# Performance work log

Hardware: AMD Instinct MI355X
Metric: run time of the kernel (lower is better)

Reference implementation:

```python
import jax, jax.numpy as jnp
import numpy as np
from jax import lax

C = 64          # in_c
D_INNER = 128   # expand=2 * C
D_STATE = 16
D_CONV = 4
DT_RANK = 4     # ceil(C/16)
B, H, W = 4, 64, 64


def setup_inputs() -> dict:
    key = jax.random.key(0)
    ks = jax.random.split(key, 22)
    def n(k, shape, s=0.05):
        return jax.random.normal(k, shape, jnp.float32) * s
    inp = {}
    inp["x"] = jax.random.normal(ks[0], (B, C, H, W), jnp.float32)
    # AxialDW: depthwise (3,1) and (1,3) convs, groups=C
    inp["dwh_w"] = n(ks[1], (C, 1, 3, 1), 0.2); inp["dwh_b"] = n(ks[2], (C,))
    inp["dww_w"] = n(ks[3], (C, 1, 1, 3), 0.2); inp["dww_b"] = n(ks[4], (C,))
    # 1x1 conv
    inp["conv_w"] = n(ks[5], (C, C, 1, 1), 0.1); inp["conv_b"] = n(ks[6], (C,))
    # BatchNorm (eval mode, running stats)
    inp["bn_g"] = jnp.ones((C,), jnp.float32); inp["bn_b"] = jnp.zeros((C,), jnp.float32)
    inp["bn_m"] = n(ks[7], (C,), 0.1)
    inp["bn_v"] = jnp.abs(n(ks[8], (C,), 0.1)) + 1.0
    # ResMambaBlock: LayerNorm + Mamba(d_model=C) + residual
    inp["ln_g"] = jnp.ones((C,), jnp.float32); inp["ln_b"] = jnp.zeros((C,), jnp.float32)
    inp["in_proj_w"] = n(ks[9], (2 * D_INNER, C))
    inp["convd_w"] = n(ks[10], (D_INNER, 1, D_CONV), 0.2); inp["convd_b"] = n(ks[11], (D_INNER,))
    inp["x_proj_w"] = n(ks[12], (DT_RANK + 2 * D_STATE, D_INNER))
    inp["dt_proj_w"] = n(ks[13], (D_INNER, DT_RANK), 0.2)
    inp["dt_proj_b"] = n(ks[14], (D_INNER,), 0.5) - 4.0  # softplus -> small dt
    inp["A_log"] = jnp.log(jnp.tile(jnp.arange(1, D_STATE + 1, dtype=jnp.float32), (D_INNER, 1)))
    inp["Dp"] = jnp.ones((D_INNER,), jnp.float32)
    inp["out_proj_w"] = n(ks[15], (C, D_INNER))
    return inp


def _mamba(h, in_proj_w, convd_w, convd_b, x_proj_w, dt_proj_w, dt_proj_b, A_log, Dp, out_proj_w):
    # h: [B, L, C]
    Bt, L, _ = h.shape
    xz = jnp.einsum('blc,dc->bld', h, in_proj_w)          # [B,L,2*D_INNER]
    xm, z = jnp.split(xz, 2, axis=-1)
    # causal depthwise conv1d over L
    xc = lax.conv_general_dilated(xm.transpose(0, 2, 1), convd_w, (1,), [(D_CONV - 1, 0)],
                                  feature_group_count=D_INNER,
                                  dimension_numbers=('NCH', 'OIH', 'NCH'))
    xc = jax.nn.silu(xc + convd_b[None, :, None]).transpose(0, 2, 1)  # [B,L,D_INNER]
    dbc = jnp.einsum('bld,ed->ble', xc, x_proj_w)
    dt, Bm, Cm = jnp.split(dbc, [DT_RANK, DT_RANK + D_STATE], axis=-1)
    dt = jax.nn.softplus(jnp.einsum('blr,dr->bld', dt, dt_proj_w) + dt_proj_b)  # [B,L,D_INNER]
    A = -jnp.exp(A_log)                                    # [D_INNER, D_STATE]
    dA = jnp.exp(dt[..., None] * A)                        # [B,L,D_INNER,D_STATE]
    dBx = dt[..., None] * Bm[:, :, None, :] * xc[..., None]  # [B,L,D_INNER,D_STATE]

    def step(hc, inp):
        dA_t, dBx_t, C_t = inp
        hc = hc * dA_t + dBx_t                             # [B,D_INNER,D_STATE]
        y = jnp.einsum('bds,bs->bd', hc, C_t)
        return hc, y

    h0 = jnp.zeros((Bt, D_INNER, D_STATE), h.dtype)
    _, ys = lax.scan(step, h0, (dA.transpose(1, 0, 2, 3), dBx.transpose(1, 0, 2, 3), Cm.transpose(1, 0, 2)))
    ys = ys.transpose(1, 0, 2)                             # [B,L,D_INNER]
    ys = (ys + xc * Dp) * jax.nn.silu(z)
    return jnp.einsum('bld,cd->blc', ys, out_proj_w)


def _forward(x, dwh_w, dwh_b, dww_w, dww_b, conv_w, conv_b, bn_g, bn_b, bn_m, bn_v,
             ln_g, ln_b, in_proj_w, convd_w, convd_b, x_proj_w, dt_proj_w, dt_proj_b,
             A_log, Dp, out_proj_w):
    dn = ('NCHW', 'OIHW', 'NCHW')
    xh = lax.conv_general_dilated(x, dwh_w, (1, 1), 'SAME', feature_group_count=C, dimension_numbers=dn)
    xw = lax.conv_general_dilated(x, dww_w, (1, 1), 'SAME', feature_group_count=C, dimension_numbers=dn)
    x = x + xh + dwh_b[None, :, None, None] + xw + dww_b[None, :, None, None]
    x = lax.conv_general_dilated(x, conv_w, (1, 1), 'SAME', dimension_numbers=dn) + conv_b[None, :, None, None]
    x = (x - bn_m[None, :, None, None]) * lax.rsqrt(bn_v + 1e-5)[None, :, None, None] \
        * bn_g[None, :, None, None] + bn_b[None, :, None, None]
    x = jax.nn.relu(x)
    # ResMambaBlock: LN + Mamba + residual over tokens [B, H*W, C]
    Bt, Cc, Hh, Ww = x.shape
    seq = x.reshape(Bt, Cc, Hh * Ww).transpose(0, 2, 1)    # [B,L,C]
    mu = seq.mean(-1, keepdims=True)
    var = ((seq - mu) ** 2).mean(-1, keepdims=True)
    hn = (seq - mu) * lax.rsqrt(var + 1e-5) * ln_g + ln_b
    y = _mamba(hn, in_proj_w, convd_w, convd_b, x_proj_w, dt_proj_w, dt_proj_b, A_log, Dp, out_proj_w)
    out = (y + seq).transpose(0, 2, 1).reshape(Bt, Cc, Hh, Ww)
    return out


def reference(x, dwh_w, dwh_b, dww_w, dww_b, conv_w, conv_b, bn_g, bn_b, bn_m, bn_v,
              ln_g, ln_b, in_proj_w, convd_w, convd_b, x_proj_w, dt_proj_w, dt_proj_b,
              A_log, Dp, out_proj_w):
    return _forward(x, dwh_w, dwh_b, dww_w, dww_b, conv_w, conv_b, bn_g, bn_b, bn_m, bn_v,
                    ln_g, ln_b, in_proj_w, convd_w, convd_b, x_proj_w, dt_proj_w, dt_proj_b,
                    A_log, Dp, out_proj_w)
```

## Files before the change

kernel.cpp:

```cpp
#include <hip/hip_runtime.h>
#include <hip/hip_bf16.h>
#include <math.h>

#define BB 4
#define CC 64
#define LL 4096
#define DI 128
#define DS 16
#define NC 64
#define CL 64

__global__ __launch_bounds__(256) void k12_front(
    const float* __restrict__ x, const float* __restrict__ dwh_w,
    const float* __restrict__ dwh_b, const float* __restrict__ dww_w,
    const float* __restrict__ dww_b, const float* __restrict__ conv_w,
    const float* __restrict__ conv_b, const float* __restrict__ bn_g,
    const float* __restrict__ bn_b, const float* __restrict__ bn_m,
    const float* __restrict__ bn_v, const float* __restrict__ ln_g,
    const float* __restrict__ ln_b, float* __restrict__ seqT,
    float* __restrict__ hn) {
  __shared__ __align__(16) float tsm[64 * 68];
  __shared__ __align__(16) float wt[64 * 68];
  __shared__ float vsm[64 * 65];
  int tid = threadIdx.x;
  int blk = blockIdx.x;
  int b = blk >> 6, h = blk & 63;
  for (int i = tid; i < 4096; i += 256) {
    int co = i >> 6, ci = i & 63;
    wt[ci * 68 + co] = conv_w[i];
  }
  for (int i = tid; i < 4096; i += 256) {
    int c = i >> 6, w = i & 63;
    int base = ((b * 64 + c) << 12) + (h << 6) + w;
    float cen = x[base];
    float up = (h > 0)  ? x[base - 64] : 0.f;
    float dn = (h < 63) ? x[base + 64] : 0.f;
    float lf = (w > 0)  ? x[base - 1]  : 0.f;
    float rt = (w < 63) ? x[base + 1]  : 0.f;
    float t = cen + dwh_w[c*3]*up + dwh_w[c*3+1]*cen + dwh_w[c*3+2]*dn + dwh_b[c]
                  + dww_w[c*3]*lf + dww_w[c*3+1]*cen + dww_w[c*3+2]*rt + dww_b[c];
    tsm[c * 68 + w] = t;
  }
  __syncthreads();
  int co0 = (tid & 15) << 2;
  int w0  = (tid >> 4) << 2;
  float acc[4][4] = {};
  #pragma unroll 8
  for (int ci = 0; ci < 64; ++ci) {
    const float4 w4 = *(const float4*)&wt[ci * 68 + co0];
    const float4 t4 = *(const float4*)&tsm[ci * 68 + w0];
    const float wv[4] = {w4.x, w4.y, w4.z, w4.w};
    const float tv[4] = {t4.x, t4.y, t4.z, t4.w};
    #pragma unroll
    for (int jc = 0; jc < 4; ++jc)
      #pragma unroll
      for (int iw = 0; iw < 4; ++iw)
        acc[jc][iw] = fmaf(wv[jc], tv[iw], acc[jc][iw]);
  }
  #pragma unroll
  for (int j = 0; j < 4; ++j) {
    int co = co0 + j;
    float sc = bn_g[co] * rsqrtf(bn_v[co] + 1e-5f);
    float sh = bn_b[co] - bn_m[co] * sc;
    float cb = conv_b[co];
    float4 o4;
    float* oo = (float*)&o4;
    #pragma unroll
    for (int i = 0; i < 4; ++i) {
      float v = fmaxf(fmaf(acc[j][i] + cb, sc, sh), 0.f);
      vsm[(w0 + i) * 65 + co] = v;
      oo[i] = v;
    }
    *(float4*)&seqT[((size_t)(b * 64 + co) << 12) + (h << 6) + w0] = o4;
  }
  __syncthreads();
  int lane = tid & 63, wv_ = tid >> 6;
  float lg = ln_g[lane], lb = ln_b[lane];
  for (int k = 0; k < 16; ++k) {
    int w = wv_ * 16 + k;
    float v = vsm[w * 65 + lane];
    float sum = v, sq = v * v;
    #pragma unroll
    for (int off = 1; off < 64; off <<= 1) {
      sum += __shfl_xor(sum, off, 64);
      sq  += __shfl_xor(sq,  off, 64);
    }
    float mu  = sum * (1.f / 64.f);
    float var = sq * (1.f / 64.f) - mu * mu;
    float inv = rsqrtf(var + 1e-5f);
    hn[((size_t)((b << 12) + (h << 6) + w) << 6) + lane] = (v - mu) * inv * lg + lb;
  }
}

__global__ __launch_bounds__(256) void k3_inproj(
    const float* __restrict__ hn, const float* __restrict__ ipw,
    float* __restrict__ xm, float* __restrict__ z) {
  __shared__ __align__(16) float wsm[64 * 132];
  __shared__ __align__(16) float hsm[64 * 68];
  int tid = threadIdx.x;
  int half = blockIdx.y;
  int blk = blockIdx.x;
  int b  = blk >> 6;
  int l0 = (blk & 63) << 6;
  const float* wsrc = ipw + half * 8192;
  for (int i = tid; i < 8192; i += 256) {
    int d = i >> 6, c = i & 63;
    wsm[c * 132 + d] = wsrc[i];
  }
  for (int i = tid; i < 4096; i += 256) {
    int t = i >> 6, c = i & 63;
    hsm[c * 68 + t] = hn[((size_t)(b * LL + l0) << 6) + i];
  }
  __syncthreads();
  int d0 = (tid & 31) << 2;
  int t0 = (tid >> 5) << 3;
  float acc[4][8] = {};
  #pragma unroll 8
  for (int c = 0; c < 64; ++c) {
    const float4 w4 = *(const float4*)&wsm[c * 132 + d0];
    const float4 h0 = *(const float4*)&hsm[c * 68 + t0];
    const float4 h1 = *(const float4*)&hsm[c * 68 + t0 + 4];
    const float wv[4] = {w4.x, w4.y, w4.z, w4.w};
    const float hv[8] = {h0.x, h0.y, h0.z, h0.w, h1.x, h1.y, h1.z, h1.w};
    #pragma unroll
    for (int i = 0; i < 4; ++i)
      #pragma unroll
      for (int j = 0; j < 8; ++j)
        acc[i][j] = fmaf(wv[i], hv[j], acc[i][j]);
  }
  float* dst = half ? z : xm;
  #pragma unroll
  for (int j = 0; j < 8; ++j) {
    float4 v = make_float4(acc[0][j], acc[1][j], acc[2][j], acc[3][j]);
    *(float4*)&dst[((size_t)(b * LL + l0 + t0 + j) << 7) + d0] = v;
  }
}

__global__ __launch_bounds__(128) void k4_conv_proj(
    const float* __restrict__ xm, const float* __restrict__ convd_w,
    const float* __restrict__ convd_b, const float* __restrict__ xpw,
    const float* __restrict__ dpw, const float* __restrict__ dpb,
    float* __restrict__ xc_g, float* __restrict__ dt_g,
    float* __restrict__ Bm_g, float* __restrict__ Cm_g) {
  __shared__ float xms[11 * 128];
  __shared__ float xcs[8 * 132];
  __shared__ float xpws[128 * 36];
  __shared__ float dbcs[8 * 36];
  int tid = threadIdx.x;
  int blk = blockIdx.x;
  int b  = blk >> 9;
  int l0 = (blk & 511) << 3;
  for (int r = 0; r < 11; ++r) {
    int l = l0 - 3 + r;
    xms[r * 128 + tid] = (l >= 0) ? xm[((size_t)(b * LL + l) << 7) + tid] : 0.f;
  }
  for (int i = tid; i < 4608; i += 128) {
    int e = i >> 7, d = i & 127;
    xpws[d * 36 + e] = xpw[i];
  }
  __syncthreads();
  float cw0 = convd_w[tid*4+0], cw1 = convd_w[tid*4+1];
  float cw2 = convd_w[tid*4+2], cw3 = convd_w[tid*4+3];
  float cb = convd_b[tid];
  #pragma unroll
  for (int t = 0; t < 8; ++t) {
    float pre = cb + cw0 * xms[t*128 + tid] + cw1 * xms[(t+1)*128 + tid]
                   + cw2 * xms[(t+2)*128 + tid] + cw3 * xms[(t+3)*128 + tid];
    float v = pre / (1.f + __expf(-pre));
    xcs[t * 132 + tid] = v;
    xc_g[((size_t)(b * LL + l0 + t) << 7) + tid] = v;
  }
  __syncthreads();
  for (int p = tid; p < 288; p += 128) {
    int t = p / 36, e = p - t * 36;
    float acc = 0.f;
    #pragma unroll
    for (int d = 0; d < 128; ++d)
      acc += xpws[d * 36 + e] * xcs[t * 132 + d];
    dbcs[t * 36 + e] = acc;
  }
  __syncthreads();
  float w0 = dpw[tid*4+0], w1 = dpw[tid*4+1], w2 = dpw[tid*4+2], w3 = dpw[tid*4+3];
  float bb = dpb[tid];
  #pragma unroll
  for (int t = 0; t < 8; ++t) {
    float raw = bb + w0 * dbcs[t*36+0] + w1 * dbcs[t*36+1]
                   + w2 * dbcs[t*36+2] + w3 * dbcs[t*36+3];
    float sp = (raw > 20.f) ? raw : log1pf(__expf(raw));
    dt_g[((size_t)(b * LL + l0 + t) << 7) + tid] = sp;
  }
  int tl = tid >> 4, s = tid & 15;
  Bm_g[((size_t)(b * LL + l0 + tl) << 4) + s] = dbcs[tl * 36 + 4 + s];
  Cm_g[((size_t)(b * LL + l0 + tl) << 4) + s] = dbcs[tl * 36 + 20 + s];
}

__global__ __launch_bounds__(128) void k5a_chunk(
    const float* __restrict__ dt_g, const float* __restrict__ Bm_g,
    const float* __restrict__ xc_g, const float* __restrict__ A_log,
    float* __restrict__ h_end, float* __restrict__ Pp) {
  int blk = blockIdx.x;
  int b = blk >> 6, ch = blk & 63;
  int d = threadIdx.x;
  int l0 = ch << 6;
  const float* dt_p = dt_g + ((size_t)b << 19);
  const float* xc_p = xc_g + ((size_t)b << 19);
  const float* Bm_p = Bm_g + ((size_t)b << 16);
  float A[16], h[16], p[16];
  #pragma unroll
  for (int q = 0; q < 4; ++q) {
    float4 a4 = *(const float4*)&A_log[d * 16 + q * 4];
    A[q*4]   = -__expf(a4.x); A[q*4+1] = -__expf(a4.y);
    A[q*4+2] = -__expf(a4.z); A[q*4+3] = -__expf(a4.w);
  }
  #pragma unroll
  for (int s = 0; s < 16; ++s) { h[s] = 0.f; p[s] = 1.f; }
  #pragma unroll 2
  for (int i = 0; i < CL; ++i) {
    int l = l0 + i;
    float dtv = dt_p[(l << 7) + d];
    float xcv = xc_p[(l << 7) + d];
    float dtx = dtv * xcv;
    float Bv[16];
    #pragma unroll
    for (int q = 0; q < 4; ++q) {
      float4 b4 = *(const float4*)&Bm_p[(l << 4) + q * 4];
      Bv[q*4] = b4.x; Bv[q*4+1] = b4.y; Bv[q*4+2] = b4.z; Bv[q*4+3] = b4.w;
    }
    #pragma unroll
    for (int s = 0; s < 16; ++s) {
      float dA = __expf(dtv * A[s]);
      h[s] = fmaf(h[s], dA, dtx * Bv[s]);
      p[s] *= dA;
    }
  }
  float* he = h_end + ((((size_t)blk << 7) + d) << 4);
  float* pe = Pp    + ((((size_t)blk << 7) + d) << 4);
  #pragma unroll
  for (int q = 0; q < 4; ++q) {
    *(float4*)&he[q * 4] = make_float4(h[q*4], h[q*4+1], h[q*4+2], h[q*4+3]);
    *(float4*)&pe[q * 4] = make_float4(p[q*4], p[q*4+1], p[q*4+2], p[q*4+3]);
  }
}

__global__ __launch_bounds__(256) void k5b_carry(
    const float* __restrict__ h_end, const float* __restrict__ Pp,
    float* __restrict__ h_in) {
  int blk = blockIdx.x;
  int b = blk >> 3;
  int r = ((blk & 7) << 8) + threadIdx.x;
  size_t o = ((size_t)b << 17) + r;
  float P0 = Pp[o], h0 = h_end[o];
  float H = 0.f;
  for (int c = 0; c < NC - 1; ++c) {
    size_t on = o + 2048;
    float Pn = Pp[on];
    float hn_ = h_end[on];
    h_in[o] = H;
    H = fmaf(H, P0, h0);
    P0 = Pn; h0 = hn_; o = on;
  }
  h_in[o] = H;
}

__global__ __launch_bounds__(256) void k56_scan_out(
    const float* __restrict__ dt_g, const float* __restrict__ Bm_g,
    const float* __restrict__ Cm_g, const float* __restrict__ xc_g,
    const float* __restrict__ A_log, const float* __restrict__ h_in,
    const float* __restrict__ z_g, const float* __restrict__ Dp,
    const float* __restrict__ opw, const float* __restrict__ seqT,
    float* __restrict__ out) {
  __shared__ __align__(16) float ysm[128 * 64];
  __shared__ __align__(16) float wsm[128 * 64];
  int tid = threadIdx.x;
  int blk = blockIdx.x;
  int b = blk >> 6, ch = blk & 63;
  int l0 = ch << 6;
  if (tid < 128) {
    int d = tid;
    const float* dt_p = dt_g + ((size_t)b << 19);
    const float* xc_p = xc_g + ((size_t)b << 19);
    const float* z_p  = z_g  + ((size_t)b << 19);
    const float* Bm_p = Bm_g + ((size_t)b << 16);
    const float* Cm_p = Cm_g + ((size_t)b << 16);
    float A[16], h[16];
    const float* hi = h_in + ((((size_t)blk << 7) + d) << 4);
    #pragma unroll
    for (int q = 0; q < 4; ++q) {
      float4 a4 = *(const float4*)&A_log[d * 16 + q * 4];
      A[q*4]   = -__expf(a4.x); A[q*4+1] = -__expf(a4.y);
      A[q*4+2] = -__expf(a4.z); A[q*4+3] = -__expf(a4.w);
      float4 h4 = *(const float4*)&hi[q * 4];
      h[q*4] = h4.x; h[q*4+1] = h4.y; h[q*4+2] = h4.z; h[q*4+3] = h4.w;
    }
    float dpv = Dp[d];
    int sw = (d & 15) << 2;
    #pragma unroll 2
    for (int i = 0; i < CL; ++i) {
      int l = l0 + i;
      float dtv = dt_p[(l << 7) + d];
      float xcv = xc_p[(l << 7) + d];
      float dtx = dtv * xcv;
      float Bv[16], Cv[16];
      #pragma unroll
      for (int q = 0; q < 4; ++q) {
        float4 b4 = *(const float4*)&Bm_p[(l << 4) + q * 4];
        float4 c4 = *(const float4*)&Cm_p[(l << 4) + q * 4];
        Bv[q*4] = b4.x; Bv[q*4+1] = b4.y; Bv[q*4+2] = b4.z; Bv[q*4+3] = b4.w;
        Cv[q*4] = c4.x; Cv[q*4+1] = c4.y; Cv[q*4+2] = c4.z; Cv[q*4+3] = c4.w;
      }
      float y = 0.f;
      #pragma unroll
      for (int s = 0; s < 16; ++s) {
        float dA = __expf(dtv * A[s]);
        h[s] = fmaf(h[s], dA, dtx * Bv[s]);
        y = fmaf(h[s], Cv[s], y);
      }
      float zz = z_p[(l << 7) + d];
      float sil = zz / (1.f + __expf(-zz));
      ysm[(d << 6) + ((i + sw) & 63)] = (y + xcv * dpv) * sil;
    }
  } else {
    for (int i = tid - 128; i < 8192; i += 128) {
      int cc = i >> 7, d = i & 127;
      wsm[(d << 6) + ((cc + ((d & 15) << 2)) & 63)] = opw[i];
    }
  }
  __syncthreads();
  int t0 = (tid >> 4) << 2;
  int c0 = (tid & 15) << 2;
  float acc[4][4] = {};
  #pragma unroll 4
  for (int d = 0; d < 128; ++d) {
    int sw = (d & 15) << 2;
    const float4 y4 = *(const float4*)&ysm[(d << 6) + ((t0 + sw) & 63)];
    const float4 w4 = *(const float4*)&wsm[(d << 6) + ((c0 + sw) & 63)];
    const float yv[4] = {y4.x, y4.y, y4.z, y4.w};
    const float wv[4] = {w4.x, w4.y, w4.z, w4.w};
    #pragma unroll
    for (int i = 0; i < 4; ++i)
      #pragma unroll
      for (int j = 0; j < 4; ++j)
        acc[i][j] = fmaf(yv[i], wv[j], acc[i][j]);
  }
  #pragma unroll
  for (int j = 0; j < 4; ++j) {
    size_t row = ((size_t)(b * 64 + c0 + j) << 12) + l0 + t0;
    float4 s4 = *(const float4*)&seqT[row];
    float4 o4 = make_float4(acc[0][j] + s4.x, acc[1][j] + s4.y,
                            acc[2][j] + s4.z, acc[3][j] + s4.w);
    *(float4*)&out[row] = o4;
  }
}

extern "C" void kernel_launch(void* const* d_in, const int* in_sizes, int n_in,
                              void* d_out, int out_size, void* d_ws, size_t ws_size,
                              hipStream_t stream) {
  const float* x       = (const float*)d_in[0];
  const float* dwh_w   = (const float*)d_in[1];
  const float* dwh_b   = (const float*)d_in[2];
  const float* dww_w   = (const float*)d_in[3];
  const float* dww_b   = (const float*)d_in[4];
  const float* conv_w  = (const float*)d_in[5];
  const float* conv_b  = (const float*)d_in[6];
  const float* bn_g    = (const float*)d_in[7];
  const float* bn_b    = (const float*)d_in[8];
  const float* bn_m    = (const float*)d_in[9];
  const float* bn_v    = (const float*)d_in[10];
  const float* ln_g    = (const float*)d_in[11];
  const float* ln_b    = (const float*)d_in[12];
  const float* ipw     = (const float*)d_in[13];
  const float* convd_w = (const float*)d_in[14];
  const float* convd_b = (const float*)d_in[15];
  const float* xpw     = (const float*)d_in[16];
  const float* dpw     = (const float*)d_in[17];
  const float* dpb     = (const float*)d_in[18];
  const float* A_log   = (const float*)d_in[19];
  const float* Dp      = (const float*)d_in[20];
  const float* opw     = (const float*)d_in[21];
  float* out = (float*)d_out;

  float* ws = (float*)d_ws;
  const size_t M = 1048576;
  const size_t K = 262144;
  float* seqT  = ws + 0;
  float* hn    = ws + M;
  float* h_end = ws + M;
  float* P_buf = ws + M + 2 * K;
  float* Bm    = ws + 2 * M;
  float* Cm    = ws + 2 * M + K;
  float* h_in  = ws + 2 * M + 2 * K;
  float* xm    = ws + 3 * M;
  float* z_buf = ws + 5 * M;
  float* xc    = ws + 7 * M;
  float* dt    = ws + 9 * M;

  k12_front<<<256, 256, 0, stream>>>(x, dwh_w, dwh_b, dww_w, dww_b, conv_w,
                                     conv_b, bn_g, bn_b, bn_m, bn_v, ln_g,
                                     ln_b, seqT, hn);
  k3_inproj<<<dim3(256, 2), 256, 0, stream>>>(hn, ipw, xm, z_buf);
  k4_conv_proj<<<2048, 128, 0, stream>>>(xm, convd_w, convd_b, xpw, dpw, dpb,
                                         xc, dt, Bm, Cm);
  k5a_chunk<<<BB * NC, 128, 0, stream>>>(dt, Bm, xc, A_log, h_end, P_buf);
  k5b_carry<<<32, 256, 0, stream>>>(h_end, P_buf, h_in);
  k56_scan_out<<<BB * NC, 256, 0, stream>>>(dt, Bm, Cm, xc, A_log, h_in,
                                            z_buf, Dp, opw, seqT, out);
}
```

Measured before the change: 224.9 us.

## Halve scan chunk length and run both halves per block in scan-out

Doubles the number of scan chunks to 128 of length 32. The chunk-summary kernel now stores its results transposed so the carry kernel reads each state's chunk sequence contiguously. The scan-out kernel keeps 64 output tiles but uses all 256 threads for the recurrence, two 32-step chunks per block, and all threads also load the out-projection weights. This shortens the serial dependency chain and doubles the active scan threads, at the cost of a longer carry loop and a larger workspace with strided stores.

```diff
diff --git a/kernel.cpp b/kernel.cpp
--- a/kernel.cpp
+++ b/kernel.cpp
@@ -7,8 +7,8 @@
 #define LL 4096
 #define DI 128
 #define DS 16
-#define NC 64
-#define CL 64
+#define NC 128
+#define CL 32
 
 __global__ __launch_bounds__(256) void k12_front(
     const float* __restrict__ x, const float* __restrict__ dwh_w,
@@ -199,9 +199,9 @@
     const float* __restrict__ xc_g, const float* __restrict__ A_log,
     float* __restrict__ h_end, float* __restrict__ Pp) {
   int blk = blockIdx.x;
-  int b = blk >> 6, ch = blk & 63;
+  int b = blk >> 7, ch = blk & (NC - 1);
   int d = threadIdx.x;
-  int l0 = ch << 6;
+  int l0 = ch << 5;
   const float* dt_p = dt_g + ((size_t)b << 19);
   const float* xc_p = xc_g + ((size_t)b << 19);
   const float* Bm_p = Bm_g + ((size_t)b << 16);
@@ -233,33 +233,29 @@
       p[s] *= dA;
     }
   }
-  float* he = h_end + ((((size_t)blk << 7) + d) << 4);
-  float* pe = Pp    + ((((size_t)blk << 7) + d) << 4);
-  #pragma unroll
-  for (int q = 0; q < 4; ++q) {
-    *(float4*)&he[q * 4] = make_float4(h[q*4], h[q*4+1], h[q*4+2], h[q*4+3]);
-    *(float4*)&pe[q * 4] = make_float4(p[q*4], p[q*4+1], p[q*4+2], p[q*4+3]);
+  size_t rbase = (((size_t)b * 2048 + (size_t)d * 16) << 7) + ch;
+  #pragma unroll
+  for (int s = 0; s < 16; ++s) {
+    h_end[rbase + ((size_t)s << 7)] = h[s];
+    Pp[rbase + ((size_t)s << 7)]    = p[s];
   }
 }
 
 __global__ __launch_bounds__(256) void k5b_carry(
     const float* __restrict__ h_end, const float* __restrict__ Pp,
     float* __restrict__ h_in) {
-  int blk = blockIdx.x;
-  int b = blk >> 3;
-  int r = ((blk & 7) << 8) + threadIdx.x;
-  size_t o = ((size_t)b << 17) + r;
-  float P0 = Pp[o], h0 = h_end[o];
+  int g = blockIdx.x * 256 + threadIdx.x;
+  int b = g >> 11;
+  int r = g & 2047;
+  const float* he = h_end + (((size_t)b * 2048 + r) << 7);
+  const float* pe = Pp    + (((size_t)b * 2048 + r) << 7);
+  float* hi = h_in + ((size_t)b << 18) + r;
   float H = 0.f;
-  for (int c = 0; c < NC - 1; ++c) {
-    size_t on = o + 2048;
-    float Pn = Pp[on];
-    float hn_ = h_end[on];
-    h_in[o] = H;
-    H = fmaf(H, P0, h0);
-    P0 = Pn; h0 = hn_; o = on;
-  }
-  h_in[o] = H;
+  #pragma unroll 4
+  for (int c = 0; c < NC; ++c) {
+    hi[(size_t)c << 11] = H;
+    H = fmaf(H, pe[c], he[c]);
+  }
 }
 
 __global__ __launch_bounds__(256) void k56_scan_out(
@@ -275,38 +271,46 @@
   int blk = blockIdx.x;
   int b = blk >> 6, ch = blk & 63;
   int l0 = ch << 6;
-  if (tid < 128) {
-    int d = tid;
+  for (int i = tid; i < 8192; i += 256) {
+    int cc = i >> 7, d = i & 127;
+    wsm[(d << 6) + ((cc + ((d & 15) << 2)) & 63)] = opw[i];
+  }
+  {
+    int q = tid >> 7;
+    int d = tid & 127;
+    int cidx = (ch << 1) + q;
+    int lc0 = cidx << 5;
     const float* dt_p = dt_g + ((size_t)b << 19);
     const float* xc_p = xc_g + ((size_t)b << 19);
     const float* z_p  = z_g  + ((size_t)b << 19);
     const float* Bm_p = Bm_g + ((size_t)b << 16);
     const float* Cm_p = Cm_g + ((size_t)b << 16);
     float A[16], h[16];
-    const float* hi = h_in + ((((size_t)blk << 7) + d) << 4);
-    #pragma unroll
-    for (int q = 0; q < 4; ++q) {
-      float4 a4 = *(const float4*)&A_log[d * 16 + q * 4];
-      A[q*4]   = -__expf(a4.x); A[q*4+1] = -__expf(a4.y);
-      A[q*4+2] = -__expf(a4.z); A[q*4+3] = -__expf(a4.w);
-      float4 h4 = *(const float4*)&hi[q * 4];
-      h[q*4] = h4.x; h[q*4+1] = h4.y; h[q*4+2] = h4.z; h[q*4+3] = h4.w;
+    const float* hi = h_in + ((size_t)b << 18) + ((size_t)cidx << 11) + (d << 4);
+    #pragma unroll
+    for (int q4 = 0; q4 < 4; ++q4) {
+      float4 a4 = *(const float4*)&A_log[d * 16 + q4 * 4];
+      A[q4*4]   = -__expf(a4.x); A[q4*4+1] = -__expf(a4.y);
+      A[q4*4+2] = -__expf(a4.z); A[q4*4+3] = -__expf(a4.w);
+      float4 h4 = *(const float4*)&hi[q4 * 4];
+      h[q4*4] = h4.x; h[q4*4+1] = h4.y; h[q4*4+2] = h4.z; h[q4*4+3] = h4.w;
     }
     float dpv = Dp[d];
     int sw = (d & 15) << 2;
+    int t_off = q << 5;
     #pragma unroll 2
     for (int i = 0; i < CL; ++i) {
-      int l = l0 + i;
+      int l = lc0 + i;
       float dtv = dt_p[(l << 7) + d];
       float xcv = xc_p[(l << 7) + d];
       float dtx = dtv * xcv;
       float Bv[16], Cv[16];
       #pragma unroll
-      for (int q = 0; q < 4; ++q) {
-        float4 b4 = *(const float4*)&Bm_p[(l << 4) + q * 4];
-        float4 c4 = *(const float4*)&Cm_p[(l << 4) + q * 4];
-        Bv[q*4] = b4.x; Bv[q*4+1] = b4.y; Bv[q*4+2] = b4.z; Bv[q*4+3] = b4.w;
-        Cv[q*4] = c4.x; Cv[q*4+1] = c4.y; Cv[q*4+2] = c4.z; Cv[q*4+3] = c4.w;
+      for (int q4 = 0; q4 < 4; ++q4) {
+        float4 b4 = *(const float4*)&Bm_p[(l << 4) + q4 * 4];
+        float4 c4 = *(const float4*)&Cm_p[(l << 4) + q4 * 4];
+        Bv[q4*4] = b4.x; Bv[q4*4+1] = b4.y; Bv[q4*4+2] = b4.z; Bv[q4*4+3] = b4.w;
+        Cv[q4*4] = c4.x; Cv[q4*4+1] = c4.y; Cv[q4*4+2] = c4.z; Cv[q4*4+3] = c4.w;
       }
       float y = 0.f;
       #pragma unroll
@@ -317,12 +321,7 @@
       }
       float zz = z_p[(l << 7) + d];
       float sil = zz / (1.f + __expf(-zz));
-      ysm[(d << 6) + ((i + sw) & 63)] = (y + xcv * dpv) * sil;
-    }
-  } else {
-    for (int i = tid - 128; i < 8192; i += 128) {
-      int cc = i >> 7, d = i & 127;
-      wsm[(d << 6) + ((cc + ((d & 15) << 2)) & 63)] = opw[i];
+      ysm[(d << 6) + ((t_off + i + sw) & 63)] = (y + xcv * dpv) * sil;
     }
   }
   __syncthreads();
@@ -385,11 +384,11 @@
   float* seqT  = ws + 0;
   float* hn    = ws + M;
   float* h_end = ws + M;
-  float* P_buf = ws + M + 2 * K;
   float* Bm    = ws + 2 * M;
   float* Cm    = ws + 2 * M + K;
-  float* h_in  = ws + 2 * M + 2 * K;
   float* xm    = ws + 3 * M;
+  float* P_buf = ws + 3 * M;
+  float* h_in  = ws + 4 * M;
   float* z_buf = ws + 5 * M;
   float* xc    = ws + 7 * M;
   float* dt    = ws + 9 * M;
@@ -402,6 +401,6 @@
                                          xc, dt, Bm, Cm);
   k5a_chunk<<<BB * NC, 128, 0, stream>>>(dt, Bm, xc, A_log, h_end, P_buf);
   k5b_carry<<<32, 256, 0, stream>>>(h_end, P_buf, h_in);
-  k56_scan_out<<<BB * NC, 256, 0, stream>>>(dt, Bm, Cm, xc, A_log, h_in,
+  k56_scan_out<<<BB * 64, 256, 0, stream>>>(dt, Bm, Cm, xc, A_log, h_in,
                                             z_buf, Dp, opw, seqT, out);
 }
```

Result: slower. 235.8 us (+4.8%).

## Fuse in_proj into front kernel and conv/x_proj into chunk scan kernel

Applied to the files above, without the earlier changes.

The front kernel now keeps the LayerNorm output in shared memory and computes both halves of the in_proj GEMM in-block, so the hn round trip through global memory and one launch go away. The depthwise conv, x_proj and dt_proj stage is merged into the chunk-scan kernel, which walks its 64-token chunk in 8-token steps and feeds dt, xc and B straight from registers and shared memory into the state recurrence. This removes two launches and the re-read of dt, B and xc from global memory. In exchange, parallelism for the conv/proj stage falls from 2048 blocks to 256 serialized blocks, and the front kernel's per-block in_proj weight loads are serialized.

```diff
diff --git a/kernel.cpp b/kernel.cpp
--- a/kernel.cpp
+++ b/kernel.cpp
@@ -10,18 +10,20 @@
 #define NC 64
 #define CL 64
 
-__global__ __launch_bounds__(256) void k12_front(
+__global__ __launch_bounds__(256) void kA_front(
     const float* __restrict__ x, const float* __restrict__ dwh_w,
     const float* __restrict__ dwh_b, const float* __restrict__ dww_w,
     const float* __restrict__ dww_b, const float* __restrict__ conv_w,
     const float* __restrict__ conv_b, const float* __restrict__ bn_g,
     const float* __restrict__ bn_b, const float* __restrict__ bn_m,
     const float* __restrict__ bn_v, const float* __restrict__ ln_g,
-    const float* __restrict__ ln_b, float* __restrict__ seqT,
-    float* __restrict__ hn) {
-  __shared__ __align__(16) float tsm[64 * 68];
-  __shared__ __align__(16) float wt[64 * 68];
-  __shared__ float vsm[64 * 65];
+    const float* __restrict__ ln_b, const float* __restrict__ ipw,
+    float* __restrict__ seqT, float* __restrict__ xm, float* __restrict__ z) {
+  __shared__ __align__(16) float smem[12864];
+  float* tsm  = smem;
+  float* wt   = smem + 4352;
+  float* vsm  = smem + 8704;
+  float* wsm2 = smem + 4352;
   int tid = threadIdx.x;
   int blk = blockIdx.x;
   int b = blk >> 6, h = blk & 63;
@@ -42,199 +44,181 @@
     tsm[c * 68 + w] = t;
   }
   __syncthreads();
-  int co0 = (tid & 15) << 2;
-  int w0  = (tid >> 4) << 2;
-  float acc[4][4] = {};
-  #pragma unroll 8
-  for (int ci = 0; ci < 64; ++ci) {
-    const float4 w4 = *(const float4*)&wt[ci * 68 + co0];
-    const float4 t4 = *(const float4*)&tsm[ci * 68 + w0];
-    const float wv[4] = {w4.x, w4.y, w4.z, w4.w};
-    const float tv[4] = {t4.x, t4.y, t4.z, t4.w};
-    #pragma unroll
-    for (int jc = 0; jc < 4; ++jc)
-      #pragma unroll
-      for (int iw = 0; iw < 4; ++iw)
-        acc[jc][iw] = fmaf(wv[jc], tv[iw], acc[jc][iw]);
-  }
-  #pragma unroll
-  for (int j = 0; j < 4; ++j) {
-    int co = co0 + j;
-    float sc = bn_g[co] * rsqrtf(bn_v[co] + 1e-5f);
-    float sh = bn_b[co] - bn_m[co] * sc;
-    float cb = conv_b[co];
-    float4 o4;
-    float* oo = (float*)&o4;
-    #pragma unroll
-    for (int i = 0; i < 4; ++i) {
-      float v = fmaxf(fmaf(acc[j][i] + cb, sc, sh), 0.f);
-      vsm[(w0 + i) * 65 + co] = v;
-      oo[i] = v;
-    }
-    *(float4*)&seqT[((size_t)(b * 64 + co) << 12) + (h << 6) + w0] = o4;
+  {
+    int co0 = (tid & 15) << 2;
+    int w0  = (tid >> 4) << 2;
+    float acc[4][4] = {};
+    #pragma unroll 8
+    for (int ci = 0; ci < 64; ++ci) {
+      const float4 w4 = *(const float4*)&wt[ci * 68 + co0];
+      const float4 t4 = *(const float4*)&tsm[ci * 68 + w0];
+      const float wv[4] = {w4.x, w4.y, w4.z, w4.w};
+      const float tv[4] = {t4.x, t4.y, t4.z, t4.w};
+      #pragma unroll
+      for (int jc = 0; jc < 4; ++jc)
+        #pragma unroll
+        for (int iw = 0; iw < 4; ++iw)
+          acc[jc][iw] = fmaf(wv[jc], tv[iw], acc[jc][iw]);
+    }
+    #pragma unroll
+    for (int j = 0; j < 4; ++j) {
+      int co = co0 + j;
+      float sc = bn_g[co] * rsqrtf(bn_v[co] + 1e-5f);
+      float sh = bn_b[co] - bn_m[co] * sc;
+      float cb = conv_b[co];
+      float4 o4;
+      float* oo = (float*)&o4;
+      #pragma unroll
+      for (int i = 0; i < 4; ++i) {
+        float v = fmaxf(fmaf(acc[j][i] + cb, sc, sh), 0.f);
+        vsm[(w0 + i) * 65 + co] = v;
+        oo[i] = v;
+      }
+      *(float4*)&seqT[((size_t)(b * 64 + co) << 12) + (h << 6) + w0] = o4;
+    }
   }
   __syncthreads();
-  int lane = tid & 63, wv_ = tid >> 6;
-  float lg = ln_g[lane], lb = ln_b[lane];
-  for (int k = 0; k < 16; ++k) {
-    int w = wv_ * 16 + k;
-    float v = vsm[w * 65 + lane];
-    float sum = v, sq = v * v;
-    #pragma unroll
-    for (int off = 1; off < 64; off <<= 1) {
-      sum += __shfl_xor(sum, off, 64);
-      sq  += __shfl_xor(sq,  off, 64);
-    }
-    float mu  = sum * (1.f / 64.f);
-    float var = sq * (1.f / 64.f) - mu * mu;
-    float inv = rsqrtf(var + 1e-5f);
-    hn[((size_t)((b << 12) + (h << 6) + w) << 6) + lane] = (v - mu) * inv * lg + lb;
-  }
-}
-
-__global__ __launch_bounds__(256) void k3_inproj(
-    const float* __restrict__ hn, const float* __restrict__ ipw,
-    float* __restrict__ xm, float* __restrict__ z) {
-  __shared__ __align__(16) float wsm[64 * 132];
-  __shared__ __align__(16) float hsm[64 * 68];
-  int tid = threadIdx.x;
-  int half = blockIdx.y;
-  int blk = blockIdx.x;
-  int b  = blk >> 6;
-  int l0 = (blk & 63) << 6;
-  const float* wsrc = ipw + half * 8192;
-  for (int i = tid; i < 8192; i += 256) {
-    int d = i >> 6, c = i & 63;
-    wsm[c * 132 + d] = wsrc[i];
-  }
-  for (int i = tid; i < 4096; i += 256) {
-    int t = i >> 6, c = i & 63;
-    hsm[c * 68 + t] = hn[((size_t)(b * LL + l0) << 6) + i];
+  {
+    int lane = tid & 63, wv_ = tid >> 6;
+    float lg = ln_g[lane], lb = ln_b[lane];
+    for (int k = 0; k < 16; ++k) {
+      int w = wv_ * 16 + k;
+      float v = vsm[w * 65 + lane];
+      float sum = v, sq = v * v;
+      #pragma unroll
+      for (int off = 1; off < 64; off <<= 1) {
+        sum += __shfl_xor(sum, off, 64);
+        sq  += __shfl_xor(sq,  off, 64);
+      }
+      float mu  = sum * (1.f / 64.f);
+      float var = sq * (1.f / 64.f) - mu * mu;
+      float inv = rsqrtf(var + 1e-5f);
+      tsm[lane * 68 + w] = (v - mu) * inv * lg + lb;
+    }
   }
   __syncthreads();
-  int d0 = (tid & 31) << 2;
-  int t0 = (tid >> 5) << 3;
-  float acc[4][8] = {};
-  #pragma unroll 8
-  for (int c = 0; c < 64; ++c) {
-    const float4 w4 = *(const float4*)&wsm[c * 132 + d0];
-    const float4 h0 = *(const float4*)&hsm[c * 68 + t0];
-    const float4 h1 = *(const float4*)&hsm[c * 68 + t0 + 4];
-    const float wv[4] = {w4.x, w4.y, w4.z, w4.w};
-    const float hv[8] = {h0.x, h0.y, h0.z, h0.w, h1.x, h1.y, h1.z, h1.w};
-    #pragma unroll
-    for (int i = 0; i < 4; ++i)
-      #pragma unroll
-      for (int j = 0; j < 8; ++j)
-        acc[i][j] = fmaf(wv[i], hv[j], acc[i][j]);
-  }
-  float* dst = half ? z : xm;
-  #pragma unroll
-  for (int j = 0; j < 8; ++j) {
-    float4 v = make_float4(acc[0][j], acc[1][j], acc[2][j], acc[3][j]);
-    *(float4*)&dst[((size_t)(b * LL + l0 + t0 + j) << 7) + d0] = v;
-  }
-}
-
-__global__ __launch_bounds__(128) void k4_conv_proj(
+  for (int half = 0; half < 2; ++half) {
+    for (int i = tid; i < 8192; i += 256) {
+      int d = i >> 6, c = i & 63;
+      wsm2[c * 132 + d] = ipw[half * 8192 + i];
+    }
+    __syncthreads();
+    int d0 = (tid & 31) << 2;
+    int t0 = (tid >> 5) << 3;
+    float acc[4][8] = {};
+    #pragma unroll 8
+    for (int c = 0; c < 64; ++c) {
+      const float4 w4 = *(const float4*)&wsm2[c * 132 + d0];
+      const float4 h0 = *(const float4*)&tsm[c * 68 + t0];
+      const float4 h1 = *(const float4*)&tsm[c * 68 + t0 + 4];
+      const float wv[4] = {w4.x, w4.y, w4.z, w4.w};
+      const float hv[8] = {h0.x, h0.y, h0.z, h0.w, h1.x, h1.y, h1.z, h1.w};
+      #pragma unroll
+      for (int i = 0; i < 4; ++i)
+        #pragma unroll
+        for (int j = 0; j < 8; ++j)
+          acc[i][j] = fmaf(wv[i], hv[j], acc[i][j]);
+    }
+    float* dst = half ? z : xm;
+    #pragma unroll
+    for (int j = 0; j < 8; ++j) {
+      float4 v = make_float4(acc[0][j], acc[1][j], acc[2][j], acc[3][j]);
+      *(float4*)&dst[((size_t)(b * LL + (h << 6) + t0 + j) << 7) + d0] = v;
+    }
+    __syncthreads();
+  }
+}
+
+__global__ __launch_bounds__(128) void kB_convscan(
     const float* __restrict__ xm, const float* __restrict__ convd_w,
     const float* __restrict__ convd_b, const float* __restrict__ xpw,
     const float* __restrict__ dpw, const float* __restrict__ dpb,
-    float* __restrict__ xc_g, float* __restrict__ dt_g,
-    float* __restrict__ Bm_g, float* __restrict__ Cm_g) {
+    const float* __restrict__ A_log, float* __restrict__ xc_g,
+    float* __restrict__ dt_g, float* __restrict__ Bm_g,
+    float* __restrict__ Cm_g, float* __restrict__ h_end,
+    float* __restrict__ Pp) {
   __shared__ float xms[11 * 128];
   __shared__ float xcs[8 * 132];
   __shared__ float xpws[128 * 36];
   __shared__ float dbcs[8 * 36];
   int tid = threadIdx.x;
   int blk = blockIdx.x;
-  int b  = blk >> 9;
-  int l0 = (blk & 511) << 3;
-  for (int r = 0; r < 11; ++r) {
-    int l = l0 - 3 + r;
-    xms[r * 128 + tid] = (l >= 0) ? xm[((size_t)(b * LL + l) << 7) + tid] : 0.f;
-  }
+  int b = blk >> 6, ch = blk & 63;
   for (int i = tid; i < 4608; i += 128) {
     int e = i >> 7, d = i & 127;
     xpws[d * 36 + e] = xpw[i];
   }
-  __syncthreads();
   float cw0 = convd_w[tid*4+0], cw1 = convd_w[tid*4+1];
   float cw2 = convd_w[tid*4+2], cw3 = convd_w[tid*4+3];
   float cb = convd_b[tid];
-  #pragma unroll
-  for (int t = 0; t < 8; ++t) {
-    float pre = cb + cw0 * xms[t*128 + tid] + cw1 * xms[(t+1)*128 + tid]
-                   + cw2 * xms[(t+2)*128 + tid] + cw3 * xms[(t+3)*128 + tid];
-    float v = pre / (1.f + __expf(-pre));
-    xcs[t * 132 + tid] = v;
-    xc_g[((size_t)(b * LL + l0 + t) << 7) + tid] = v;
-  }
-  __syncthreads();
-  for (int p = tid; p < 288; p += 128) {
-    int t = p / 36, e = p - t * 36;
-    float acc = 0.f;
-    #pragma unroll
-    for (int d = 0; d < 128; ++d)
-      acc += xpws[d * 36 + e] * xcs[t * 132 + d];
-    dbcs[t * 36 + e] = acc;
-  }
-  __syncthreads();
   float w0 = dpw[tid*4+0], w1 = dpw[tid*4+1], w2 = dpw[tid*4+2], w3 = dpw[tid*4+3];
   float bb = dpb[tid];
-  #pragma unroll
-  for (int t = 0; t < 8; ++t) {
-    float raw = bb + w0 * dbcs[t*36+0] + w1 * dbcs[t*36+1]
-                   + w2 * dbcs[t*36+2] + w3 * dbcs[t*36+3];
-    float sp = (raw > 20.f) ? raw : log1pf(__expf(raw));
-    dt_g[((size_t)(b * LL + l0 + t) << 7) + tid] = sp;
-  }
-  int tl = tid >> 4, s = tid & 15;
-  Bm_g[((size_t)(b * LL + l0 + tl) << 4) + s] = dbcs[tl * 36 + 4 + s];
-  Cm_g[((size_t)(b * LL + l0 + tl) << 4) + s] = dbcs[tl * 36 + 20 + s];
-}
-
-__global__ __launch_bounds__(128) void k5a_chunk(
-    const float* __restrict__ dt_g, const float* __restrict__ Bm_g,
-    const float* __restrict__ xc_g, const float* __restrict__ A_log,
-    float* __restrict__ h_end, float* __restrict__ Pp) {
-  int blk = blockIdx.x;
-  int b = blk >> 6, ch = blk & 63;
-  int d = threadIdx.x;
-  int l0 = ch << 6;
-  const float* dt_p = dt_g + ((size_t)b << 19);
-  const float* xc_p = xc_g + ((size_t)b << 19);
-  const float* Bm_p = Bm_g + ((size_t)b << 16);
   float A[16], h[16], p[16];
   #pragma unroll
   for (int q = 0; q < 4; ++q) {
-    float4 a4 = *(const float4*)&A_log[d * 16 + q * 4];
+    float4 a4 = *(const float4*)&A_log[tid * 16 + q * 4];
     A[q*4]   = -__expf(a4.x); A[q*4+1] = -__expf(a4.y);
     A[q*4+2] = -__expf(a4.z); A[q*4+3] = -__expf(a4.w);
   }
   #pragma unroll
   for (int s = 0; s < 16; ++s) { h[s] = 0.f; p[s] = 1.f; }
-  #pragma unroll 2
-  for (int i = 0; i < CL; ++i) {
-    int l = l0 + i;
-    float dtv = dt_p[(l << 7) + d];
-    float xcv = xc_p[(l << 7) + d];
-    float dtx = dtv * xcv;
-    float Bv[16];
-    #pragma unroll
-    for (int q = 0; q < 4; ++q) {
-      float4 b4 = *(const float4*)&Bm_p[(l << 4) + q * 4];
-      Bv[q*4] = b4.x; Bv[q*4+1] = b4.y; Bv[q*4+2] = b4.z; Bv[q*4+3] = b4.w;
-    }
-    #pragma unroll
-    for (int s = 0; s < 16; ++s) {
-      float dA = __expf(dtv * A[s]);
-      h[s] = fmaf(h[s], dA, dtx * Bv[s]);
-      p[s] *= dA;
-    }
-  }
-  float* he = h_end + ((((size_t)blk << 7) + d) << 4);
-  float* pe = Pp    + ((((size_t)blk << 7) + d) << 4);
+  for (int st = 0; st < 8; ++st) {
+    int l0s = (ch << 6) + (st << 3);
+    __syncthreads();
+    for (int r = 0; r < 11; ++r) {
+      int l = l0s - 3 + r;
+      xms[r * 128 + tid] = (l >= 0) ? xm[((size_t)(b * LL + l) << 7) + tid] : 0.f;
+    }
+    __syncthreads();
+    float xc_t[8];
+    #pragma unroll
+    for (int t = 0; t < 8; ++t) {
+      float pre = cb + cw0 * xms[t*128 + tid] + cw1 * xms[(t+1)*128 + tid]
+                     + cw2 * xms[(t+2)*128 + tid] + cw3 * xms[(t+3)*128 + tid];
+      float v = pre / (1.f + __expf(-pre));
+      xcs[t * 132 + tid] = v;
+      xc_t[t] = v;
+      xc_g[((size_t)(b * LL + l0s + t) << 7) + tid] = v;
+    }
+    __syncthreads();
+    for (int pp = tid; pp < 288; pp += 128) {
+      int t = pp / 36, e = pp - t * 36;
+      float acc = 0.f;
+      #pragma unroll
+      for (int d = 0; d < 128; ++d)
+        acc += xpws[d * 36 + e] * xcs[t * 132 + d];
+      dbcs[t * 36 + e] = acc;
+    }
+    __syncthreads();
+    float dt_t[8];
+    #pragma unroll
+    for (int t = 0; t < 8; ++t) {
+      float raw = bb + w0 * dbcs[t*36+0] + w1 * dbcs[t*36+1]
+                     + w2 * dbcs[t*36+2] + w3 * dbcs[t*36+3];
+      float sp = (raw > 20.f) ? raw : log1pf(__expf(raw));
+      dt_t[t] = sp;
+      dt_g[((size_t)(b * LL + l0s + t) << 7) + tid] = sp;
+    }
+    {
+      int tl = tid >> 4, s = tid & 15;
+      Bm_g[((size_t)(b * LL + l0s + tl) << 4) + s] = dbcs[tl * 36 + 4 + s];
+      Cm_g[((size_t)(b * LL + l0s + tl) << 4) + s] = dbcs[tl * 36 + 20 + s];
+    }
+    #pragma unroll
+    for (int i = 0; i < 8; ++i) {
+      float dtv = dt_t[i];
+      float dtx = dtv * xc_t[i];
+      #pragma unroll
+      for (int s = 0; s < 16; ++s) {
+        float Bv = dbcs[i * 36 + 4 + s];
+        float dA = __expf(dtv * A[s]);
+        h[s] = fmaf(h[s], dA, dtx * Bv);
+        p[s] *= dA;
+      }
+    }
+  }
+  float* he = h_end + ((((size_t)blk << 7) + tid) << 4);
+  float* pe = Pp    + ((((size_t)blk << 7) + tid) << 4);
   #pragma unroll
   for (int q = 0; q < 4; ++q) {
     *(float4*)&he[q * 4] = make_float4(h[q*4], h[q*4+1], h[q*4+2], h[q*4+3]);
@@ -302,11 +286,11 @@
       float dtx = dtv * xcv;
       float Bv[16], Cv[16];
       #pragma unroll
-      for (int q = 0; q < 4; ++q) {
-        float4 b4 = *(const float4*)&Bm_p[(l << 4) + q * 4];
-        float4 c4 = *(const float4*)&Cm_p[(l << 4) + q * 4];
-        Bv[q*4] = b4.x; Bv[q*4+1] = b4.y; Bv[q*4+2] = b4.z; Bv[q*4+3] = b4.w;
-        Cv[q*4] = c4.x; Cv[q*4+1] = c4.y; Cv[q*4+2] = c4.z; Cv[q*4+3] = c4.w;
+      for (int q4 = 0; q4 < 4; ++q4) {
+        float4 b4 = *(const float4*)&Bm_p[(l << 4) + q4 * 4];
+        float4 c4 = *(const float4*)&Cm_p[(l << 4) + q4 * 4];
+        Bv[q4*4] = b4.x; Bv[q4*4+1] = b4.y; Bv[q4*4+2] = b4.z; Bv[q4*4+3] = b4.w;
+        Cv[q4*4] = c4.x; Cv[q4*4+1] = c4.y; Cv[q4*4+2] = c4.z; Cv[q4*4+3] = c4.w;
       }
       float y = 0.f;
       #pragma unroll
@@ -383,24 +367,22 @@
   const size_t M = 1048576;
   const size_t K = 262144;
   float* seqT  = ws + 0;
-  float* hn    = ws + M;
-  float* h_end = ws + M;
-  float* P_buf = ws + M + 2 * K;
-  float* Bm    = ws + 2 * M;
-  float* Cm    = ws + 2 * M + K;
-  float* h_in  = ws + 2 * M + 2 * K;
-  float* xm    = ws + 3 * M;
-  float* z_buf = ws + 5 * M;
-  float* xc    = ws + 7 * M;
-  float* dt    = ws + 9 * M;
-
-  k12_front<<<256, 256, 0, stream>>>(x, dwh_w, dwh_b, dww_w, dww_b, conv_w,
-                                     conv_b, bn_g, bn_b, bn_m, bn_v, ln_g,
-                                     ln_b, seqT, hn);
-  k3_inproj<<<dim3(256, 2), 256, 0, stream>>>(hn, ipw, xm, z_buf);
-  k4_conv_proj<<<2048, 128, 0, stream>>>(xm, convd_w, convd_b, xpw, dpw, dpb,
-                                         xc, dt, Bm, Cm);
-  k5a_chunk<<<BB * NC, 128, 0, stream>>>(dt, Bm, xc, A_log, h_end, P_buf);
+  float* xm    = ws + M;
+  float* z_buf = ws + 3 * M;
+  float* xc    = ws + 5 * M;
+  float* dt    = ws + 7 * M;
+  float* Bm    = ws + 9 * M;
+  float* Cm    = ws + 9 * M + K;
+  float* h_end = ws + 9 * M + 2 * K;
+  float* P_buf = ws + 10 * M;
+  float* h_in  = ws + 10 * M + 2 * K;
+
+  kA_front<<<256, 256, 0, stream>>>(x, dwh_w, dwh_b, dww_w, dww_b, conv_w,
+                                    conv_b, bn_g, bn_b, bn_m, bn_v, ln_g,
+                                    ln_b, ipw, seqT, xm, z_buf);
+  kB_convscan<<<BB * NC, 128, 0, stream>>>(xm, convd_w, convd_b, xpw, dpw,
+                                           dpb, A_log, xc, dt, Bm, Cm,
+                                           h_end, P_buf);
   k5b_carry<<<32, 256, 0, stream>>>(h_end, P_buf, h_in);
   k56_scan_out<<<BB * NC, 256, 0, stream>>>(dt, Bm, Cm, xc, A_log, h_in,
                                             z_buf, Dp, opw, seqT, out);
```

Result: slower. 257.0 us (+14.2%).
